# Performance work log

Hardware: AMD Instinct MI355X
Metric: run time of the kernel (lower is better)

## Reference

```python
import jax, jax.numpy as jnp
import numpy as np

DIM = 1024
MEM_DIM = 1024
BANK = 8192
B, S = 4, 4096
LN_EPS = 1e-5


def setup_inputs() -> dict:
    key = jax.random.key(0)
    ks = jax.random.split(key, 8)
    std_q = 1.0 / np.sqrt(DIM)
    std_m = 1.0 / np.sqrt(MEM_DIM)
    std_f = 1.0 / np.sqrt(DIM + MEM_DIM)
    return {
        "x": jax.random.normal(ks[0], (B, S, DIM), jnp.float32),
        "knowledge_bank": 0.02 * jax.random.normal(ks[1], (BANK, MEM_DIM), jnp.float32),
        "wq": std_q * jax.random.normal(ks[2], (MEM_DIM, DIM), jnp.float32),
        "bq": jnp.zeros((MEM_DIM,), jnp.float32),
        "wk": std_m * jax.random.normal(ks[3], (MEM_DIM, MEM_DIM), jnp.float32),
        "bk": jnp.zeros((MEM_DIM,), jnp.float32),
        "wv": std_m * jax.random.normal(ks[4], (DIM, MEM_DIM), jnp.float32),
        "bv": jnp.zeros((DIM,), jnp.float32),
        "wf": std_f * jax.random.normal(ks[5], (DIM, DIM + MEM_DIM), jnp.float32),
        "bf": jnp.zeros((DIM,), jnp.float32),
        "gamma": jnp.ones((DIM,), jnp.float32),
        "beta": jnp.zeros((DIM,), jnp.float32),
    }


def reference(x, knowledge_bank, wq, bq, wk, bk, wv, bv, wf, bf, gamma, beta):
    # queries: [B,S,MEM_DIM]; keys/values over the fixed bank: [BANK, *]
    queries = jnp.einsum("bsd,md->bsm", x, wq) + bq
    keys = jnp.einsum("nd,md->nm", knowledge_bank, wk) + bk
    values = jnp.einsum("nd,md->nm", knowledge_bank, wv) + bv
    scores = jnp.einsum("bsm,nm->bsn", queries, keys) / jnp.sqrt(
        jnp.asarray(MEM_DIM, x.dtype)
    )
    attn = jax.nn.softmax(scores, axis=-1)  # [B,S,BANK]
    retrieved = jnp.einsum("bsn,nd->bsd", attn, values)  # [B,S,DIM]
    combined = jnp.concatenate([x, retrieved], axis=-1)  # [B,S,2*DIM]
    out = jnp.einsum("bsc,dc->bsd", combined, wf) + bf
    h = out + x
    # LayerNorm over last dim, eps = 1e-5 (torch default)
    mu = jnp.mean(h, axis=-1, keepdims=True)
    var = jnp.mean(jnp.square(h - mu), axis=-1, keepdims=True)
    return (h - mu) * jax.lax.rsqrt(var + LN_EPS) * gamma + beta
```

## Files before the change

kernel.cpp:

```cpp
#include <hip/hip_runtime.h>


typedef __bf16 bf16;
typedef __bf16 bf16x4 __attribute__((ext_vector_type(4)));
typedef __bf16 bf16x8 __attribute__((ext_vector_type(8)));
typedef float f32x4 __attribute__((ext_vector_type(4)));

static __device__ __forceinline__ f32x4 mfma16(bf16x8 a, bf16x8 b, f32x4 c) {
  return __builtin_amdgcn_mfma_f32_16x16x32_bf16(a, b, c, 0, 0, 0);
}

#define GLDS16(gp, lp) __builtin_amdgcn_global_load_lds( \
    (const __attribute__((address_space(1))) void*)(gp), \
    (__attribute__((address_space(3))) void*)(lp), 16, 0, 0)

template<int EPI, int CONCAT>
__global__ __launch_bounds__(256, 3) void gemm_bb(
    const bf16* __restrict__ A, const bf16* __restrict__ A2,
    const bf16* __restrict__ W, const float* __restrict__ bias,
    const float* __restrict__ resid, float* __restrict__ L,
    void* __restrict__ Cout, int N, int K)
{
  __shared__ bf16 As[128 * 64];
  __shared__ bf16 Bs[128 * 64];
  const int tid = threadIdx.x, lane = tid & 63, wid = tid >> 6;
  const int wm = (wid >> 1) * 64, wn = (wid & 1) * 64;
  const int quad = lane >> 4, l16 = lane & 15;
  const long bm = (long)blockIdx.y * 128, bn = (long)blockIdx.x * 128;

  int prow[4], pcg[4];
#pragma unroll
  for (int i = 0; i < 4; ++i) {
    int p = ((wid * 4 + i) << 6) + lane;
    prow[i] = p >> 3;
    pcg[i] = (p & 7) ^ (prow[i] & 7);
  }

  f32x4 acc[4][4] = {};

  for (int k0 = 0; k0 < K; k0 += 64) {
    const bf16* Asrc = (CONCAT && k0 >= 1024) ? A2 : A;
    const int kA = (CONCAT && k0 >= 1024) ? k0 - 1024 : k0;
    const int lda = CONCAT ? 1024 : K;
    __syncthreads();
#pragma unroll
    for (int i = 0; i < 4; ++i) {
      const bf16* ga = Asrc + (size_t)(bm + prow[i]) * lda + kA + pcg[i] * 8;
      GLDS16(ga, (char*)As + ((wid * 4 + i) << 10));
    }
#pragma unroll
    for (int i = 0; i < 4; ++i) {
      const bf16* gb = W + (size_t)(bn + prow[i]) * K + k0 + pcg[i] * 8;
      GLDS16(gb, (char*)Bs + ((wid * 4 + i) << 10));
    }
    __syncthreads();
#pragma unroll
    for (int kk = 0; kk < 2; ++kk) {
      bf16x8 af[4], bfv[4];
#pragma unroll
      for (int mt = 0; mt < 4; ++mt) {
        const int r = wm + mt * 16 + l16;
        af[mt] = *(const bf16x8*)((const char*)As + (r << 7)
                                  + ((((kk << 2) + quad) ^ (r & 7)) << 4));
      }
#pragma unroll
      for (int nt = 0; nt < 4; ++nt) {
        const int r = wn + nt * 16 + l16;
        bfv[nt] = *(const bf16x8*)((const char*)Bs + (r << 7)
                                   + ((((kk << 2) + quad) ^ (r & 7)) << 4));
      }
#pragma unroll
      for (int mt = 0; mt < 4; ++mt)
#pragma unroll
        for (int nt = 0; nt < 4; ++nt)
          acc[mt][nt] = mfma16(af[mt], bfv[nt], acc[mt][nt]);
    }
  }

#pragma unroll
  for (int mt = 0; mt < 4; ++mt) {
    const long row0 = bm + wm + mt * 16 + quad * 4;
    if (EPI == 2) {
      float rsum[4] = {0.f, 0.f, 0.f, 0.f};
#pragma unroll
      for (int nt = 0; nt < 4; ++nt) {
        const long col = bn + wn + nt * 16 + l16;
#pragma unroll
        for (int r = 0; r < 4; ++r) {
          float p = __expf(acc[mt][nt][r] * 0.03125f);
          rsum[r] += p;
          ((bf16*)Cout)[(size_t)(row0 + r) * N + col] = (bf16)p;
        }
      }
#pragma unroll
      for (int s = 1; s < 16; s <<= 1)
#pragma unroll
        for (int r = 0; r < 4; ++r) rsum[r] += __shfl_xor(rsum[r], s, 64);
      if (l16 == 0) {
#pragma unroll
        for (int r = 0; r < 4; ++r) atomicAdd(&L[row0 + r], rsum[r]);
      }
    } else {
#pragma unroll
      for (int nt = 0; nt < 4; ++nt) {
        const long col = bn + wn + nt * 16 + l16;
        const float bc = (EPI == 1) ? 0.f : bias[col];
#pragma unroll
        for (int r = 0; r < 4; ++r) {
          float v = acc[mt][nt][r] + ((EPI == 1) ? bias[row0 + r] : bc);
          if (EPI == 3) {
            v += resid[(size_t)(row0 + r) * 1024 + col];
            ((float*)Cout)[(size_t)(row0 + r) * N + col] = v;
          } else {
            ((bf16*)Cout)[(size_t)(row0 + r) * N + col] = (bf16)v;
          }
        }
      }
    }
  }
}

__global__ __launch_bounds__(512, 2) void pv_gemm(
    const bf16* __restrict__ P, const bf16* __restrict__ Vt,
    const float* __restrict__ L, bf16* __restrict__ Rb)
{
  __shared__ bf16 As[128 * 128];
  __shared__ bf16 Bs[128 * 128];
  const int tid = threadIdx.x, lane = tid & 63, wid = tid >> 6;
  const int wm = (wid & 3) * 32, wn = (wid >> 2) * 64;
  const int quad = lane >> 4, l16 = lane & 15;
  const long bm = (long)blockIdx.y * 128, bn = (long)blockIdx.x * 128;

  int prow[4], pcg[4];
#pragma unroll
  for (int i = 0; i < 4; ++i) {
    int p = ((wid * 4 + i) << 6) + lane;
    prow[i] = p >> 4;
    pcg[i] = (p & 15) ^ (prow[i] & 15);
  }

  f32x4 acc[2][4] = {};

  for (int k0 = 0; k0 < 8192; k0 += 128) {
    __syncthreads();
#pragma unroll
    for (int i = 0; i < 4; ++i)
      GLDS16(P + (size_t)(bm + prow[i]) * 8192 + k0 + pcg[i] * 8,
             (char*)As + ((wid * 4 + i) << 10));
#pragma unroll
    for (int i = 0; i < 4; ++i)
      GLDS16(Vt + (size_t)(bn + prow[i]) * 8192 + k0 + pcg[i] * 8,
             (char*)Bs + ((wid * 4 + i) << 10));
    __syncthreads();
#pragma unroll
    for (int kk = 0; kk < 4; ++kk) {
      bf16x8 af[2], bfv[4];
#pragma unroll
      for (int mt = 0; mt < 2; ++mt) {
        const int r = wm + mt * 16 + l16;
        af[mt] = *(const bf16x8*)((const char*)As + (r << 8)
                                  + ((((kk << 2) + quad) ^ (r & 15)) << 4));
      }
#pragma unroll
      for (int nt = 0; nt < 4; ++nt) {
        const int r = wn + nt * 16 + l16;
        bfv[nt] = *(const bf16x8*)((const char*)Bs + (r << 8)
                                   + ((((kk << 2) + quad) ^ (r & 15)) << 4));
      }
#pragma unroll
      for (int mt = 0; mt < 2; ++mt)
#pragma unroll
        for (int nt = 0; nt < 4; ++nt)
          acc[mt][nt] = mfma16(af[mt], bfv[nt], acc[mt][nt]);
    }
  }

#pragma unroll
  for (int mt = 0; mt < 2; ++mt) {
    const long row0 = bm + wm + mt * 16 + quad * 4;
    float linv[4];
#pragma unroll
    for (int r = 0; r < 4; ++r) linv[r] = 1.f / L[row0 + r];
#pragma unroll
    for (int nt = 0; nt < 4; ++nt) {
      const long col = bn + wn + nt * 16 + l16;
#pragma unroll
      for (int r = 0; r < 4; ++r)
        Rb[(size_t)(row0 + r) * 1024 + col] = (bf16)(acc[mt][nt][r] * linv[r]);
    }
  }
}

template<int BIAS_ROW, int OUT_F32_RES, int CONCAT>
__global__ __launch_bounds__(256, 3) void gemm_nt(
    const float* __restrict__ A, const bf16* __restrict__ A2,
    const float* __restrict__ W, const float* __restrict__ bias,
    const float* __restrict__ resid, void* __restrict__ Cout,
    int M, int N, int K)
{
  __shared__ bf16 As[128][72];
  __shared__ bf16 Bs[128][72];
  const int tid  = threadIdx.x;
  const int lane = tid & 63;
  const int wid  = tid >> 6;
  const int wm   = (wid >> 1) * 64, wn = (wid & 1) * 64;
  const int quad = lane >> 4, l16 = lane & 15;
  const long bm = (long)blockIdx.y * 128, bn = (long)blockIdx.x * 128;
  const int r0 = tid >> 2, cq = (tid & 3) * 16;
  const int lda = CONCAT ? 1024 : K;

  f32x4 acc[4][4] = {};

  for (int k0 = 0; k0 < K; k0 += 64) {
    const bool useb = CONCAT && (k0 >= 1024);
    const int kA = useb ? (k0 - 1024) : k0;
    f32x4 va[2][4], vb[2][4];
    bf16x8 ra[2][2];
    if (useb) {
#pragma unroll
      for (int g = 0; g < 2; ++g) {
        const bf16* p = A2 + (size_t)(bm + r0 + 64 * g) * 1024 + kA + cq;
        ra[g][0] = *(const bf16x8*)p;
        ra[g][1] = *(const bf16x8*)(p + 8);
      }
    } else {
#pragma unroll
      for (int g = 0; g < 2; ++g) {
        const f32x4* p = (const f32x4*)(A + (size_t)(bm + r0 + 64 * g) * lda + kA + cq);
#pragma unroll
        for (int j = 0; j < 4; ++j) va[g][j] = p[j];
      }
    }
#pragma unroll
    for (int g = 0; g < 2; ++g) {
      const f32x4* p = (const f32x4*)(W + (size_t)(bn + r0 + 64 * g) * K + k0 + cq);
#pragma unroll
      for (int j = 0; j < 4; ++j) vb[g][j] = p[j];
    }
    __syncthreads();
#pragma unroll
    for (int g = 0; g < 2; ++g) {
      bf16* dA = &As[r0 + 64 * g][cq];
      if (useb) {
        *(bf16x8*)dA = ra[g][0]; *(bf16x8*)(dA + 8) = ra[g][1];
      } else {
        bf16x8 t0, t1;
#pragma unroll
        for (int j = 0; j < 4; ++j) {
          t0[j] = (bf16)va[g][0][j]; t0[4 + j] = (bf16)va[g][1][j];
          t1[j] = (bf16)va[g][2][j]; t1[4 + j] = (bf16)va[g][3][j];
        }
        *(bf16x8*)dA = t0; *(bf16x8*)(dA + 8) = t1;
      }
      bf16* dB = &Bs[r0 + 64 * g][cq];
      bf16x8 u0, u1;
#pragma unroll
      for (int j = 0; j < 4; ++j) {
        u0[j] = (bf16)vb[g][0][j]; u0[4 + j] = (bf16)vb[g][1][j];
        u1[j] = (bf16)vb[g][2][j]; u1[4 + j] = (bf16)vb[g][3][j];
      }
      *(bf16x8*)dB = u0; *(bf16x8*)(dB + 8) = u1;
    }
    __syncthreads();
#pragma unroll
    for (int kk = 0; kk < 2; ++kk) {
      bf16x8 af[4], bfv[4];
#pragma unroll
      for (int mt = 0; mt < 4; ++mt)
        af[mt] = *(const bf16x8*)&As[wm + mt * 16 + l16][kk * 32 + quad * 8];
#pragma unroll
      for (int nt = 0; nt < 4; ++nt)
        bfv[nt] = *(const bf16x8*)&Bs[wn + nt * 16 + l16][kk * 32 + quad * 8];
#pragma unroll
      for (int mt = 0; mt < 4; ++mt)
#pragma unroll
        for (int nt = 0; nt < 4; ++nt)
          acc[mt][nt] = mfma16(af[mt], bfv[nt], acc[mt][nt]);
    }
  }
#pragma unroll
  for (int mt = 0; mt < 4; ++mt) {
    const long row0 = bm + wm + mt * 16 + quad * 4;
#pragma unroll
    for (int nt = 0; nt < 4; ++nt) {
      const long col = bn + wn + nt * 16 + l16;
      const float bc = BIAS_ROW ? 0.f : bias[col];
#pragma unroll
      for (int r = 0; r < 4; ++r) {
        float v = acc[mt][nt][r] + (BIAS_ROW ? bias[row0 + r] : bc);
        if (OUT_F32_RES) {
          v += resid[(size_t)(row0 + r) * 1024 + col];
          ((float*)Cout)[(size_t)(row0 + r) * N + col] = v;
        } else {
          ((bf16*)Cout)[(size_t)(row0 + r) * N + col] = (bf16)v;
        }
      }
    }
  }
}

__global__ __launch_bounds__(256) void cvt6(
    const float* __restrict__ x, const float* __restrict__ bank,
    const float* __restrict__ wq, const float* __restrict__ wk,
    const float* __restrict__ wv, const float* __restrict__ wf,
    bf16* __restrict__ xb, bf16* __restrict__ bankb,
    bf16* __restrict__ wqb, bf16* __restrict__ wkb,
    bf16* __restrict__ wvb, bf16* __restrict__ wfb)
{
  long i4 = (long)blockIdx.x * 256 + threadIdx.x;
  const float* src; bf16* dst; long off;
  if      (i4 < 4194304) { src = x;    dst = xb;    off = i4; }
  else if (i4 < 6291456) { src = bank; dst = bankb; off = i4 - 4194304; }
  else if (i4 < 6553600) { src = wq;   dst = wqb;   off = i4 - 6291456; }
  else if (i4 < 6815744) { src = wk;   dst = wkb;   off = i4 - 6553600; }
  else if (i4 < 7077888) { src = wv;   dst = wvb;   off = i4 - 6815744; }
  else if (i4 < 7602176) { src = wf;   dst = wfb;   off = i4 - 7077888; }
  else return;
  f32x4 v = ((const f32x4*)src)[off];
  bf16x4 o;
#pragma unroll
  for (int j = 0; j < 4; ++j) o[j] = (bf16)v[j];
  ((bf16x4*)dst)[off] = o;
}

__global__ __launch_bounds__(256) void zerof(float* __restrict__ p) {
  p[(size_t)blockIdx.x * 256 + threadIdx.x] = 0.f;
}

__global__ __launch_bounds__(256) void ln_kernel(
    float* __restrict__ h, const float* __restrict__ g, const float* __restrict__ b)
{
  const int tid = threadIdx.x;
  const size_t row = blockIdx.x;
  f32x4 v = *(f32x4*)&h[row * 1024 + tid * 4];
  float s1 = v[0] + v[1] + v[2] + v[3];
  float s2 = v[0]*v[0] + v[1]*v[1] + v[2]*v[2] + v[3]*v[3];
#pragma unroll
  for (int d = 1; d < 64; d <<= 1) { s1 += __shfl_xor(s1, d, 64); s2 += __shfl_xor(s2, d, 64); }
  __shared__ float a1[4], a2[4];
  const int wid = tid >> 6;
  if ((tid & 63) == 0) { a1[wid] = s1; a2[wid] = s2; }
  __syncthreads();
  s1 = a1[0] + a1[1] + a1[2] + a1[3];
  s2 = a2[0] + a2[1] + a2[2] + a2[3];
  const float mu = s1 * (1.f / 1024.f);
  const float rs = rsqrtf(s2 * (1.f / 1024.f) - mu * mu + 1e-5f);
  f32x4 gv = *(const f32x4*)&g[tid * 4];
  f32x4 bv = *(const f32x4*)&b[tid * 4];
#pragma unroll
  for (int j = 0; j < 4; ++j) v[j] = (v[j] - mu) * rs * gv[j] + bv[j];
  *(f32x4*)&h[row * 1024 + tid * 4] = v;
}

extern "C" void kernel_launch(void* const* d_in, const int* in_sizes, int n_in,
                              void* d_out, int out_size, void* d_ws, size_t ws_size,
                              hipStream_t stream)
{
  const float* x     = (const float*)d_in[0];
  const float* kbank = (const float*)d_in[1];
  const float* wq    = (const float*)d_in[2];
  const float* bq    = (const float*)d_in[3];
  const float* wk    = (const float*)d_in[4];
  const float* bk    = (const float*)d_in[5];
  const float* wv    = (const float*)d_in[6];
  const float* bv    = (const float*)d_in[7];
  const float* wf    = (const float*)d_in[8];
  const float* bf_   = (const float*)d_in[9];
  const float* gamma = (const float*)d_in[10];
  const float* beta  = (const float*)d_in[11];

  char* ws = (char*)d_ws;
  const size_t MB = 1024 * 1024;
  bf16*  Qb    = (bf16*)ws;
  bf16*  Rb    = Qb;
  bf16*  Kb    = (bf16*)(ws + 32 * MB);
  bf16*  Vt    = (bf16*)(ws + 48 * MB);
  float* L     = (float*)(ws + 64 * MB);
  bf16*  xb    = (bf16*)(ws + 65 * MB);
  bf16*  bankb = (bf16*)(ws + 97 * MB);
  bf16*  wfb   = (bf16*)(ws + 113 * MB);
  bf16*  wqb   = (bf16*)(ws + 117 * MB);
  bf16*  wkb   = (bf16*)(ws + 119 * MB);
  bf16*  wvb   = (bf16*)(ws + 121 * MB);
  bf16*  P     = (bf16*)d_out;
  float* out   = (float*)d_out;
  const bool big = ws_size >= 123 * MB;

  if (big) {
    cvt6<<<dim3(29696), dim3(256), 0, stream>>>(
        x, kbank, wq, wk, wv, wf, xb, bankb, wqb, wkb, wvb, wfb);
    gemm_bb<0,0><<<dim3(8, 128), dim3(256), 0, stream>>>(
        xb, nullptr, wqb, bq, nullptr, nullptr, (void*)Qb, 1024, 1024);
    gemm_bb<0,0><<<dim3(8, 64), dim3(256), 0, stream>>>(
        bankb, nullptr, wkb, bk, nullptr, nullptr, (void*)Kb, 1024, 1024);
    gemm_bb<1,0><<<dim3(64, 8), dim3(256), 0, stream>>>(
        wvb, nullptr, bankb, bv, nullptr, nullptr, (void*)Vt, 8192, 1024);
  } else {
    gemm_nt<0,0,0><<<dim3(8, 128), dim3(256), 0, stream>>>(
        x, nullptr, wq, bq, nullptr, (void*)Qb, 16384, 1024, 1024);
    gemm_nt<0,0,0><<<dim3(8, 64), dim3(256), 0, stream>>>(
        kbank, nullptr, wk, bk, nullptr, (void*)Kb, 8192, 1024, 1024);
    gemm_nt<1,0,0><<<dim3(64, 8), dim3(256), 0, stream>>>(
        wv, nullptr, kbank, bv, nullptr, (void*)Vt, 1024, 8192, 1024);
  }

  zerof<<<dim3(64), dim3(256), 0, stream>>>(L);
  for (int c = 0; c < 4; ++c) {
    gemm_bb<2,0><<<dim3(64, 32), dim3(256), 0, stream>>>(
        Qb + (size_t)c * 4096 * 1024, nullptr, Kb, nullptr, nullptr,
        L + c * 4096, (void*)P, 8192, 1024);
    pv_gemm<<<dim3(8, 32), dim3(512), 0, stream>>>(
        P, Vt, L + c * 4096, Rb + (size_t)c * 4096 * 1024);
  }

  if (big) {
    gemm_bb<3,1><<<dim3(8, 128), dim3(256), 0, stream>>>(
        xb, Rb, wfb, bf_, x, nullptr, (void*)out, 1024, 2048);
  } else {
    gemm_nt<0,1,1><<<dim3(8, 128), dim3(256), 0, stream>>>(
        x, Rb, wf, bf_, x, (void*)out, 16384, 1024, 2048);
  }
  ln_kernel<<<dim3(16384), dim3(256), 0, stream>>>(out, gamma, beta);
}
```

Measured before the change: 1.166 ms.

## Add 4-stage pipelined GEMM for attention and read fp32 x directly in projections

Replaces the QK and PV attention GEMMs with a new 512-thread kernel that keeps four LDS stages in flight, using explicit vmcnt waits and a single barrier per k-step so global-to-LDS loads overlap MFMA work. Removes the conversion of x to bf16. The Q and final projections now load fp32 x tiles into LDS and convert them to bf16 in registers, which drops the xb write and re-read. Deletes the small-workspace fallback path. In exchange the new kernel uses a large LDS footprint (one block per CU) and relies on hand-tuned waitcnt encodings.

```diff
diff --git a/kernel.cpp b/kernel.cpp
--- a/kernel.cpp
+++ b/kernel.cpp
@@ -14,12 +14,122 @@
     (const __attribute__((address_space(1))) void*)(gp), \
     (__attribute__((address_space(3))) void*)(lp), 16, 0, 0)
 
-template<int EPI, int CONCAT>
+#define WAIT_VM8   0xF78
+#define WAIT_VM4   0xF74
+#define WAIT_VM0   0xF70
+#define WAIT_LGKM0 0xC07F
+
+template<int EPI>
+__global__ __launch_bounds__(512, 1) void gemm_pl(
+    const bf16* __restrict__ A, const bf16* __restrict__ W,
+    float* __restrict__ L, bf16* __restrict__ C, int N, int K)
+{
+  __shared__ bf16 SA[4][128 * 64];
+  __shared__ bf16 SB[4][128 * 64];
+  const int tid = threadIdx.x, lane = tid & 63, wid = tid >> 6;
+  const int wm = (wid & 3) * 32, wn = (wid >> 2) * 64;
+  const int quad = lane >> 4, l16 = lane & 15;
+  const long bm = (long)blockIdx.y * 128, bn = (long)blockIdx.x * 128;
+
+  int arow[2], acg[2];
+#pragma unroll
+  for (int i = 0; i < 2; ++i) {
+    int p = ((wid * 2 + i) << 6) + lane;
+    arow[i] = p >> 3;
+    acg[i] = (p & 7) ^ (arow[i] & 7);
+  }
+  const int NIT = K >> 6;
+
+  f32x4 acc[2][4] = {};
+
+  auto stage = [&](int s, int buf) {
+    const int k0 = s << 6;
+#pragma unroll
+    for (int i = 0; i < 2; ++i)
+      GLDS16(A + (size_t)(bm + arow[i]) * K + k0 + acg[i] * 8,
+             (char*)SA[buf] + ((wid * 2 + i) << 10));
+#pragma unroll
+    for (int i = 0; i < 2; ++i)
+      GLDS16(W + (size_t)(bn + arow[i]) * K + k0 + acg[i] * 8,
+             (char*)SB[buf] + ((wid * 2 + i) << 10));
+  };
+  auto compute = [&](int buf) {
+#pragma unroll
+    for (int kk = 0; kk < 2; ++kk) {
+      bf16x8 af[2], bv[4];
+#pragma unroll
+      for (int mt = 0; mt < 2; ++mt) {
+        const int r = wm + mt * 16 + l16;
+        af[mt] = *(const bf16x8*)((const char*)SA[buf] + (r << 7)
+                                  + ((((kk << 2) + quad) ^ (r & 7)) << 4));
+      }
+#pragma unroll
+      for (int nt = 0; nt < 4; ++nt) {
+        const int r = wn + nt * 16 + l16;
+        bv[nt] = *(const bf16x8*)((const char*)SB[buf] + (r << 7)
+                                  + ((((kk << 2) + quad) ^ (r & 7)) << 4));
+      }
+#pragma unroll
+      for (int mt = 0; mt < 2; ++mt)
+#pragma unroll
+        for (int nt = 0; nt < 4; ++nt)
+          acc[mt][nt] = mfma16(af[mt], bv[nt], acc[mt][nt]);
+    }
+  };
+
+  stage(0, 0); stage(1, 1); stage(2, 2);
+  for (int k = 0; k < NIT; ++k) {
+    if (k < NIT - 2)       __builtin_amdgcn_s_waitcnt(WAIT_VM8);
+    else if (k == NIT - 2) __builtin_amdgcn_s_waitcnt(WAIT_VM4);
+    else                   __builtin_amdgcn_s_waitcnt(WAIT_VM0);
+    __builtin_amdgcn_s_waitcnt(WAIT_LGKM0);
+    __builtin_amdgcn_s_barrier();
+    if (k + 3 < NIT) stage(k + 3, (k + 3) & 3);
+    compute(k & 3);
+  }
+
+#pragma unroll
+  for (int mt = 0; mt < 2; ++mt) {
+    const long row0 = bm + wm + mt * 16 + quad * 4;
+    if (EPI == 0) {
+      float rsum[4] = {0.f, 0.f, 0.f, 0.f};
+#pragma unroll
+      for (int nt = 0; nt < 4; ++nt) {
+        const long col = bn + wn + nt * 16 + l16;
+#pragma unroll
+        for (int r = 0; r < 4; ++r) {
+          float p = __expf(acc[mt][nt][r] * 0.03125f);
+          rsum[r] += p;
+          C[(size_t)(row0 + r) * N + col] = (bf16)p;
+        }
+      }
+#pragma unroll
+      for (int s = 1; s < 16; s <<= 1)
+#pragma unroll
+        for (int r = 0; r < 4; ++r) rsum[r] += __shfl_xor(rsum[r], s, 64);
+      if (l16 == 0) {
+#pragma unroll
+        for (int r = 0; r < 4; ++r) atomicAdd(&L[row0 + r], rsum[r]);
+      }
+    } else {
+      float linv[4];
+#pragma unroll
+      for (int r = 0; r < 4; ++r) linv[r] = 1.f / L[row0 + r];
+#pragma unroll
+      for (int nt = 0; nt < 4; ++nt) {
+        const long col = bn + wn + nt * 16 + l16;
+#pragma unroll
+        for (int r = 0; r < 4; ++r)
+          C[(size_t)(row0 + r) * N + col] = (bf16)(acc[mt][nt][r] * linv[r]);
+      }
+    }
+  }
+}
+
+template<int EPI>
 __global__ __launch_bounds__(256, 3) void gemm_bb(
-    const bf16* __restrict__ A, const bf16* __restrict__ A2,
-    const bf16* __restrict__ W, const float* __restrict__ bias,
-    const float* __restrict__ resid, float* __restrict__ L,
-    void* __restrict__ Cout, int N, int K)
+    const bf16* __restrict__ A, const bf16* __restrict__ W,
+    const float* __restrict__ bias, bf16* __restrict__ C, int N, int K)
 {
   __shared__ bf16 As[128 * 64];
   __shared__ bf16 Bs[128 * 64];
@@ -39,20 +149,15 @@
   f32x4 acc[4][4] = {};
 
   for (int k0 = 0; k0 < K; k0 += 64) {
-    const bf16* Asrc = (CONCAT && k0 >= 1024) ? A2 : A;
-    const int kA = (CONCAT && k0 >= 1024) ? k0 - 1024 : k0;
-    const int lda = CONCAT ? 1024 : K;
     __syncthreads();
 #pragma unroll
-    for (int i = 0; i < 4; ++i) {
-      const bf16* ga = Asrc + (size_t)(bm + prow[i]) * lda + kA + pcg[i] * 8;
-      GLDS16(ga, (char*)As + ((wid * 4 + i) << 10));
-    }
-#pragma unroll
-    for (int i = 0; i < 4; ++i) {
-      const bf16* gb = W + (size_t)(bn + prow[i]) * K + k0 + pcg[i] * 8;
-      GLDS16(gb, (char*)Bs + ((wid * 4 + i) << 10));
-    }
+    for (int i = 0; i < 4; ++i)
+      GLDS16(A + (size_t)(bm + prow[i]) * K + k0 + pcg[i] * 8,
+             (char*)As + ((wid * 4 + i) << 10));
+#pragma unroll
+    for (int i = 0; i < 4; ++i)
+      GLDS16(W + (size_t)(bn + prow[i]) * K + k0 + pcg[i] * 8,
+             (char*)Bs + ((wid * 4 + i) << 10));
     __syncthreads();
 #pragma unroll
     for (int kk = 0; kk < 2; ++kk) {
@@ -80,95 +185,95 @@
 #pragma unroll
   for (int mt = 0; mt < 4; ++mt) {
     const long row0 = bm + wm + mt * 16 + quad * 4;
-    if (EPI == 2) {
-      float rsum[4] = {0.f, 0.f, 0.f, 0.f};
-#pragma unroll
-      for (int nt = 0; nt < 4; ++nt) {
-        const long col = bn + wn + nt * 16 + l16;
-#pragma unroll
-        for (int r = 0; r < 4; ++r) {
-          float p = __expf(acc[mt][nt][r] * 0.03125f);
-          rsum[r] += p;
-          ((bf16*)Cout)[(size_t)(row0 + r) * N + col] = (bf16)p;
-        }
-      }
-#pragma unroll
-      for (int s = 1; s < 16; s <<= 1)
-#pragma unroll
-        for (int r = 0; r < 4; ++r) rsum[r] += __shfl_xor(rsum[r], s, 64);
-      if (l16 == 0) {
-#pragma unroll
-        for (int r = 0; r < 4; ++r) atomicAdd(&L[row0 + r], rsum[r]);
-      }
-    } else {
-#pragma unroll
-      for (int nt = 0; nt < 4; ++nt) {
-        const long col = bn + wn + nt * 16 + l16;
-        const float bc = (EPI == 1) ? 0.f : bias[col];
-#pragma unroll
-        for (int r = 0; r < 4; ++r) {
-          float v = acc[mt][nt][r] + ((EPI == 1) ? bias[row0 + r] : bc);
-          if (EPI == 3) {
-            v += resid[(size_t)(row0 + r) * 1024 + col];
-            ((float*)Cout)[(size_t)(row0 + r) * N + col] = v;
-          } else {
-            ((bf16*)Cout)[(size_t)(row0 + r) * N + col] = (bf16)v;
-          }
-        }
-      }
-    }
-  }
-}
-
-__global__ __launch_bounds__(512, 2) void pv_gemm(
-    const bf16* __restrict__ P, const bf16* __restrict__ Vt,
-    const float* __restrict__ L, bf16* __restrict__ Rb)
-{
-  __shared__ bf16 As[128 * 128];
-  __shared__ bf16 Bs[128 * 128];
+#pragma unroll
+    for (int nt = 0; nt < 4; ++nt) {
+      const long col = bn + wn + nt * 16 + l16;
+      const float bc = (EPI == 1) ? 0.f : bias[col];
+#pragma unroll
+      for (int r = 0; r < 4; ++r) {
+        float v = acc[mt][nt][r] + ((EPI == 1) ? bias[row0 + r] : bc);
+        C[(size_t)(row0 + r) * N + col] = (bf16)v;
+      }
+    }
+  }
+}
+
+template<int EPI>
+__global__ __launch_bounds__(256, 3) void gemm_fb(
+    const float* __restrict__ A, const bf16* __restrict__ A2,
+    const bf16* __restrict__ W, const float* __restrict__ bias,
+    const float* __restrict__ resid, void* __restrict__ Cout, int N, int K)
+{
+  __shared__ float Af[128 * 64];
+  __shared__ bf16 Bs[128 * 64];
   const int tid = threadIdx.x, lane = tid & 63, wid = tid >> 6;
-  const int wm = (wid & 3) * 32, wn = (wid >> 2) * 64;
+  const int wm = (wid >> 1) * 64, wn = (wid & 1) * 64;
   const int quad = lane >> 4, l16 = lane & 15;
   const long bm = (long)blockIdx.y * 128, bn = (long)blockIdx.x * 128;
 
+  int frow[8], fg[8];
+#pragma unroll
+  for (int i = 0; i < 8; ++i) {
+    int p = ((wid * 8 + i) << 6) + lane;
+    frow[i] = p >> 4;
+    fg[i] = (p & 15) ^ (frow[i] & 15);
+  }
   int prow[4], pcg[4];
 #pragma unroll
   for (int i = 0; i < 4; ++i) {
     int p = ((wid * 4 + i) << 6) + lane;
-    prow[i] = p >> 4;
-    pcg[i] = (p & 15) ^ (prow[i] & 15);
-  }
-
-  f32x4 acc[2][4] = {};
-
-  for (int k0 = 0; k0 < 8192; k0 += 128) {
+    prow[i] = p >> 3;
+    pcg[i] = (p & 7) ^ (prow[i] & 7);
+  }
+
+  f32x4 acc[4][4] = {};
+
+  for (int k0 = 0; k0 < K; k0 += 64) {
+    const bool ph2 = (EPI == 1) && (k0 >= 1024);
     __syncthreads();
+    if (!ph2) {
+#pragma unroll
+      for (int i = 0; i < 8; ++i)
+        GLDS16(A + (size_t)(bm + frow[i]) * 1024 + k0 + fg[i] * 4,
+               (char*)Af + ((wid * 8 + i) << 10));
+    } else {
+#pragma unroll
+      for (int i = 0; i < 4; ++i)
+        GLDS16(A2 + (size_t)(bm + prow[i]) * 1024 + (k0 - 1024) + pcg[i] * 8,
+               (char*)Af + ((wid * 4 + i) << 10));
+    }
 #pragma unroll
     for (int i = 0; i < 4; ++i)
-      GLDS16(P + (size_t)(bm + prow[i]) * 8192 + k0 + pcg[i] * 8,
-             (char*)As + ((wid * 4 + i) << 10));
-#pragma unroll
-    for (int i = 0; i < 4; ++i)
-      GLDS16(Vt + (size_t)(bn + prow[i]) * 8192 + k0 + pcg[i] * 8,
+      GLDS16(W + (size_t)(bn + prow[i]) * K + k0 + pcg[i] * 8,
              (char*)Bs + ((wid * 4 + i) << 10));
     __syncthreads();
 #pragma unroll
-    for (int kk = 0; kk < 4; ++kk) {
-      bf16x8 af[2], bfv[4];
-#pragma unroll
-      for (int mt = 0; mt < 2; ++mt) {
+    for (int kk = 0; kk < 2; ++kk) {
+      bf16x8 af[4], bfv[4];
+#pragma unroll
+      for (int mt = 0; mt < 4; ++mt) {
         const int r = wm + mt * 16 + l16;
-        af[mt] = *(const bf16x8*)((const char*)As + (r << 8)
-                                  + ((((kk << 2) + quad) ^ (r & 15)) << 4));
+        if (!ph2) {
+          const int g0 = kk * 8 + quad * 2;
+          f32x4 lo = *(const f32x4*)((const char*)Af + (r << 8)
+                                     + ((g0 ^ (r & 15)) << 4));
+          f32x4 hi = *(const f32x4*)((const char*)Af + (r << 8)
+                                     + (((g0 + 1) ^ (r & 15)) << 4));
+#pragma unroll
+          for (int j = 0; j < 4; ++j) { af[mt][j] = (bf16)lo[j]; af[mt][4 + j] = (bf16)hi[j]; }
+        } else {
+          af[mt] = *(const bf16x8*)((const char*)Af + (r << 7)
+                                    + ((((kk << 2) + quad) ^ (r & 7)) << 4));
+        }
       }
 #pragma unroll
       for (int nt = 0; nt < 4; ++nt) {
         const int r = wn + nt * 16 + l16;
-        bfv[nt] = *(const bf16x8*)((const char*)Bs + (r << 8)
-                                   + ((((kk << 2) + quad) ^ (r & 15)) << 4));
-      }
-#pragma unroll
-      for (int mt = 0; mt < 2; ++mt)
+        bfv[nt] = *(const bf16x8*)((const char*)Bs + (r << 7)
+                                   + ((((kk << 2) + quad) ^ (r & 7)) << 4));
+      }
+#pragma unroll
+      for (int mt = 0; mt < 4; ++mt)
 #pragma unroll
         for (int nt = 0; nt < 4; ++nt)
           acc[mt][nt] = mfma16(af[mt], bfv[nt], acc[mt][nt]);
@@ -176,119 +281,16 @@
   }
 
 #pragma unroll
-  for (int mt = 0; mt < 2; ++mt) {
+  for (int mt = 0; mt < 4; ++mt) {
     const long row0 = bm + wm + mt * 16 + quad * 4;
-    float linv[4];
-#pragma unroll
-    for (int r = 0; r < 4; ++r) linv[r] = 1.f / L[row0 + r];
 #pragma unroll
     for (int nt = 0; nt < 4; ++nt) {
       const long col = bn + wn + nt * 16 + l16;
-#pragma unroll
-      for (int r = 0; r < 4; ++r)
-        Rb[(size_t)(row0 + r) * 1024 + col] = (bf16)(acc[mt][nt][r] * linv[r]);
-    }
-  }
-}
-
-template<int BIAS_ROW, int OUT_F32_RES, int CONCAT>
-__global__ __launch_bounds__(256, 3) void gemm_nt(
-    const float* __restrict__ A, const bf16* __restrict__ A2,
-    const float* __restrict__ W, const float* __restrict__ bias,
-    const float* __restrict__ resid, void* __restrict__ Cout,
-    int M, int N, int K)
-{
-  __shared__ bf16 As[128][72];
-  __shared__ bf16 Bs[128][72];
-  const int tid  = threadIdx.x;
-  const int lane = tid & 63;
-  const int wid  = tid >> 6;
-  const int wm   = (wid >> 1) * 64, wn = (wid & 1) * 64;
-  const int quad = lane >> 4, l16 = lane & 15;
-  const long bm = (long)blockIdx.y * 128, bn = (long)blockIdx.x * 128;
-  const int r0 = tid >> 2, cq = (tid & 3) * 16;
-  const int lda = CONCAT ? 1024 : K;
-
-  f32x4 acc[4][4] = {};
-
-  for (int k0 = 0; k0 < K; k0 += 64) {
-    const bool useb = CONCAT && (k0 >= 1024);
-    const int kA = useb ? (k0 - 1024) : k0;
-    f32x4 va[2][4], vb[2][4];
-    bf16x8 ra[2][2];
-    if (useb) {
-#pragma unroll
-      for (int g = 0; g < 2; ++g) {
-        const bf16* p = A2 + (size_t)(bm + r0 + 64 * g) * 1024 + kA + cq;
-        ra[g][0] = *(const bf16x8*)p;
-        ra[g][1] = *(const bf16x8*)(p + 8);
-      }
-    } else {
-#pragma unroll
-      for (int g = 0; g < 2; ++g) {
-        const f32x4* p = (const f32x4*)(A + (size_t)(bm + r0 + 64 * g) * lda + kA + cq);
-#pragma unroll
-        for (int j = 0; j < 4; ++j) va[g][j] = p[j];
-      }
-    }
-#pragma unroll
-    for (int g = 0; g < 2; ++g) {
-      const f32x4* p = (const f32x4*)(W + (size_t)(bn + r0 + 64 * g) * K + k0 + cq);
-#pragma unroll
-      for (int j = 0; j < 4; ++j) vb[g][j] = p[j];
-    }
-    __syncthreads();
-#pragma unroll
-    for (int g = 0; g < 2; ++g) {
-      bf16* dA = &As[r0 + 64 * g][cq];
-      if (useb) {
-        *(bf16x8*)dA = ra[g][0]; *(bf16x8*)(dA + 8) = ra[g][1];
-      } else {
-        bf16x8 t0, t1;
-#pragma unroll
-        for (int j = 0; j < 4; ++j) {
-          t0[j] = (bf16)va[g][0][j]; t0[4 + j] = (bf16)va[g][1][j];
-          t1[j] = (bf16)va[g][2][j]; t1[4 + j] = (bf16)va[g][3][j];
-        }
-        *(bf16x8*)dA = t0; *(bf16x8*)(dA + 8) = t1;
-      }
-      bf16* dB = &Bs[r0 + 64 * g][cq];
-      bf16x8 u0, u1;
-#pragma unroll
-      for (int j = 0; j < 4; ++j) {
-        u0[j] = (bf16)vb[g][0][j]; u0[4 + j] = (bf16)vb[g][1][j];
-        u1[j] = (bf16)vb[g][2][j]; u1[4 + j] = (bf16)vb[g][3][j];
-      }
-      *(bf16x8*)dB = u0; *(bf16x8*)(dB + 8) = u1;
-    }
-    __syncthreads();
-#pragma unroll
-    for (int kk = 0; kk < 2; ++kk) {
-      bf16x8 af[4], bfv[4];
-#pragma unroll
-      for (int mt = 0; mt < 4; ++mt)
-        af[mt] = *(const bf16x8*)&As[wm + mt * 16 + l16][kk * 32 + quad * 8];
-#pragma unroll
-      for (int nt = 0; nt < 4; ++nt)
-        bfv[nt] = *(const bf16x8*)&Bs[wn + nt * 16 + l16][kk * 32 + quad * 8];
-#pragma unroll
-      for (int mt = 0; mt < 4; ++mt)
-#pragma unroll
-        for (int nt = 0; nt < 4; ++nt)
-          acc[mt][nt] = mfma16(af[mt], bfv[nt], acc[mt][nt]);
-    }
-  }
-#pragma unroll
-  for (int mt = 0; mt < 4; ++mt) {
-    const long row0 = bm + wm + mt * 16 + quad * 4;
-#pragma unroll
-    for (int nt = 0; nt < 4; ++nt) {
-      const long col = bn + wn + nt * 16 + l16;
-      const float bc = BIAS_ROW ? 0.f : bias[col];
+      const float bc = bias[col];
 #pragma unroll
       for (int r = 0; r < 4; ++r) {
-        float v = acc[mt][nt][r] + (BIAS_ROW ? bias[row0 + r] : bc);
-        if (OUT_F32_RES) {
+        float v = acc[mt][nt][r] + bc;
+        if (EPI == 1) {
           v += resid[(size_t)(row0 + r) * 1024 + col];
           ((float*)Cout)[(size_t)(row0 + r) * N + col] = v;
         } else {
@@ -299,23 +301,20 @@
   }
 }
 
-__global__ __launch_bounds__(256) void cvt6(
-    const float* __restrict__ x, const float* __restrict__ bank,
-    const float* __restrict__ wq, const float* __restrict__ wk,
-    const float* __restrict__ wv, const float* __restrict__ wf,
-    bf16* __restrict__ xb, bf16* __restrict__ bankb,
+__global__ __launch_bounds__(256) void cvt5(
+    const float* __restrict__ bank, const float* __restrict__ wq,
+    const float* __restrict__ wk, const float* __restrict__ wv,
+    const float* __restrict__ wf, bf16* __restrict__ bankb,
     bf16* __restrict__ wqb, bf16* __restrict__ wkb,
     bf16* __restrict__ wvb, bf16* __restrict__ wfb)
 {
   long i4 = (long)blockIdx.x * 256 + threadIdx.x;
   const float* src; bf16* dst; long off;
-  if      (i4 < 4194304) { src = x;    dst = xb;    off = i4; }
-  else if (i4 < 6291456) { src = bank; dst = bankb; off = i4 - 4194304; }
-  else if (i4 < 6553600) { src = wq;   dst = wqb;   off = i4 - 6291456; }
-  else if (i4 < 6815744) { src = wk;   dst = wkb;   off = i4 - 6553600; }
-  else if (i4 < 7077888) { src = wv;   dst = wvb;   off = i4 - 6815744; }
-  else if (i4 < 7602176) { src = wf;   dst = wfb;   off = i4 - 7077888; }
-  else return;
+  if      (i4 < 2097152) { src = bank; dst = bankb; off = i4; }
+  else if (i4 < 2359296) { src = wq;   dst = wqb;   off = i4 - 2097152; }
+  else if (i4 < 2621440) { src = wk;   dst = wkb;   off = i4 - 2359296; }
+  else if (i4 < 2883584) { src = wv;   dst = wvb;   off = i4 - 2621440; }
+  else                   { src = wf;   dst = wfb;   off = i4 - 2883584; }
   f32x4 v = ((const f32x4*)src)[off];
   bf16x4 o;
 #pragma unroll
@@ -376,49 +375,33 @@
   bf16*  Kb    = (bf16*)(ws + 32 * MB);
   bf16*  Vt    = (bf16*)(ws + 48 * MB);
   float* L     = (float*)(ws + 64 * MB);
-  bf16*  xb    = (bf16*)(ws + 65 * MB);
-  bf16*  bankb = (bf16*)(ws + 97 * MB);
-  bf16*  wfb   = (bf16*)(ws + 113 * MB);
-  bf16*  wqb   = (bf16*)(ws + 117 * MB);
-  bf16*  wkb   = (bf16*)(ws + 119 * MB);
-  bf16*  wvb   = (bf16*)(ws + 121 * MB);
+  bf16*  wqb   = (bf16*)(ws + 65 * MB);
+  bf16*  wkb   = (bf16*)(ws + 67 * MB);
+  bf16*  wvb   = (bf16*)(ws + 69 * MB);
+  bf16*  wfb   = (bf16*)(ws + 71 * MB);
+  bf16*  bankb = (bf16*)(ws + 75 * MB);
   bf16*  P     = (bf16*)d_out;
   float* out   = (float*)d_out;
-  const bool big = ws_size >= 123 * MB;
-
-  if (big) {
-    cvt6<<<dim3(29696), dim3(256), 0, stream>>>(
-        x, kbank, wq, wk, wv, wf, xb, bankb, wqb, wkb, wvb, wfb);
-    gemm_bb<0,0><<<dim3(8, 128), dim3(256), 0, stream>>>(
-        xb, nullptr, wqb, bq, nullptr, nullptr, (void*)Qb, 1024, 1024);
-    gemm_bb<0,0><<<dim3(8, 64), dim3(256), 0, stream>>>(
-        bankb, nullptr, wkb, bk, nullptr, nullptr, (void*)Kb, 1024, 1024);
-    gemm_bb<1,0><<<dim3(64, 8), dim3(256), 0, stream>>>(
-        wvb, nullptr, bankb, bv, nullptr, nullptr, (void*)Vt, 8192, 1024);
-  } else {
-    gemm_nt<0,0,0><<<dim3(8, 128), dim3(256), 0, stream>>>(
-        x, nullptr, wq, bq, nullptr, (void*)Qb, 16384, 1024, 1024);
-    gemm_nt<0,0,0><<<dim3(8, 64), dim3(256), 0, stream>>>(
-        kbank, nullptr, wk, bk, nullptr, (void*)Kb, 8192, 1024, 1024);
-    gemm_nt<1,0,0><<<dim3(64, 8), dim3(256), 0, stream>>>(
-        wv, nullptr, kbank, bv, nullptr, (void*)Vt, 1024, 8192, 1024);
-  }
+
+  cvt5<<<dim3(13312), dim3(256), 0, stream>>>(
+      kbank, wq, wk, wv, wf, bankb, wqb, wkb, wvb, wfb);
+
+  gemm_fb<0><<<dim3(8, 128), dim3(256), 0, stream>>>(
+      x, nullptr, wqb, bq, nullptr, (void*)Qb, 1024, 1024);
+  gemm_bb<0><<<dim3(8, 64), dim3(256), 0, stream>>>(
+      bankb, wkb, bk, Kb, 1024, 1024);
+  gemm_bb<1><<<dim3(64, 8), dim3(256), 0, stream>>>(
+      wvb, bankb, bv, Vt, 8192, 1024);
 
   zerof<<<dim3(64), dim3(256), 0, stream>>>(L);
   for (int c = 0; c < 4; ++c) {
-    gemm_bb<2,0><<<dim3(64, 32), dim3(256), 0, stream>>>(
-        Qb + (size_t)c * 4096 * 1024, nullptr, Kb, nullptr, nullptr,
-        L + c * 4096, (void*)P, 8192, 1024);
-    pv_gemm<<<dim3(8, 32), dim3(512), 0, stream>>>(
-        P, Vt, L + c * 4096, Rb + (size_t)c * 4096 * 1024);
-  }
-
-  if (big) {
-    gemm_bb<3,1><<<dim3(8, 128), dim3(256), 0, stream>>>(
-        xb, Rb, wfb, bf_, x, nullptr, (void*)out, 1024, 2048);
-  } else {
-    gemm_nt<0,1,1><<<dim3(8, 128), dim3(256), 0, stream>>>(
-        x, Rb, wf, bf_, x, (void*)out, 16384, 1024, 2048);
-  }
+    gemm_pl<0><<<dim3(64, 32), dim3(512), 0, stream>>>(
+        Qb + (size_t)c * 4096 * 1024, Kb, L + c * 4096, P, 8192, 1024);
+    gemm_pl<1><<<dim3(8, 32), dim3(512), 0, stream>>>(
+        P, Vt, L + c * 4096, Rb + (size_t)c * 4096 * 1024, 1024, 8192);
+  }
+
+  gemm_fb<1><<<dim3(8, 128), dim3(256), 0, stream>>>(
+      x, Rb, wfb, bf_, x, (void*)out, 1024, 2048);
   ln_kernel<<<dim3(16384), dim3(256), 0, stream>>>(out, gamma, beta);
 }
```

After: 1.593 ms. 1.37x slower.
